# Performance work log

Measured on AMD Instinct MI355X. Metric: run time of the kernel, lower is better.

The kernel has to match this reference:

```python
import jax, jax.numpy as jnp
import numpy as np

N = 1048576        # number of raw proposals
NC = 2             # num classes (source hardcodes self.nc = 2)
CONF_THRES = 0.25  # score_thres
IOU_THRES = 0.45
MAX_WH = 4096.0    # class offset for class-aware NMS (agnostic=False)
MAX_NMS = 30000    # cap on boxes entering NMS
MAX_DET = 300      # cap on detections returned


def setup_inputs() -> dict:
    key = jax.random.key(0)
    k1, k2, k3, k4 = jax.random.split(key, 4)
    xy = jax.random.uniform(k1, (1, N, 2), dtype=jnp.float32) * 640.0          # box centers (pixels)
    wh = jax.random.uniform(k2, (1, N, 2), dtype=jnp.float32) * 98.0 + 2.0     # widths/heights in [2, 100]
    obj = jax.random.uniform(k3, (1, N, 1), dtype=jnp.float32)                 # objectness
    cls = jax.random.uniform(k4, (1, N, NC), dtype=jnp.float32)                # class scores
    prediction = jnp.concatenate([xy, wh, obj, cls], axis=-1)                  # [1, N, 4+1+nc]
    return {"prediction": prediction}


def reference(prediction):
    # Single image (source only ever fills/returns output[0]).
    pred = prediction[0]                        # [N, 7]
    obj = pred[:, 4]                            # objectness
    cls = pred[:, 5:5 + NC] * obj[:, None]      # conf = obj * cls  (nc > 1 branch)
    conf = jnp.max(cls, axis=-1)                # best-class confidence
    j = jnp.argmax(cls, axis=-1)                # best-class index

    # xywh -> xyxy
    xy, wh = pred[:, :2], pred[:, 2:4]
    box = jnp.concatenate([xy - wh * 0.5, xy + wh * 0.5], axis=-1)  # [N, 4]

    # candidate mask: obj > thres (xc) AND best-class conf > thres
    valid = (obj > CONF_THRES) & (conf > CONF_THRES)
    scores = jnp.where(valid, conf, -1.0)

    # n > max_nms: keep top MAX_NMS by confidence (argsort descending truncation)
    top_s, top_i = jax.lax.top_k(scores, MAX_NMS)       # [MAX_NMS]
    box_t = box[top_i]                                   # [MAX_NMS, 4]
    conf_t = conf[top_i]
    j_t = j[top_i]

    # class-aware NMS: offset boxes per class so classes never suppress each other
    boxes_off = box_t + (j_t.astype(box_t.dtype) * MAX_WH)[:, None]
    area = (boxes_off[:, 2] - boxes_off[:, 0]) * (boxes_off[:, 3] - boxes_off[:, 1])

    # Greedy NMS: iteratively select max-score box, suppress IoU > thres.
    # Selecting the argmax each step is equivalent to sorted greedy NMS, and
    # MAX_DET steps yields exactly the first max_det kept indices.
    def step(s, _):
        idx = jnp.argmax(s)
        ok = s[idx] > 0.0                       # any real candidate left?
        b = boxes_off[idx]
        lt = jnp.maximum(b[:2], boxes_off[:, :2])
        rb = jnp.minimum(b[2:], boxes_off[:, 2:])
        inter = jnp.prod(jnp.clip(rb - lt, 0.0), axis=-1)
        iou = inter / (area[idx] + area - inter)
        s = jnp.where(ok & (iou > IOU_THRES), -1.0, s)  # suppress (incl. self, IoU=1)
        return s, (idx, ok)

    _, (sel, ok) = jax.lax.scan(step, top_s, None, length=MAX_DET)

    dets = jnp.concatenate(
        [box_t[sel], conf_t[sel, None], j_t[sel, None].astype(box_t.dtype)], axis=-1
    )                                           # [MAX_DET, 6] = [xyxy, conf, cls]
    dets = dets * ok[:, None].astype(dets.dtype)  # zero out padding rows
    return dets, ok
```

## Files before the change

kernel.cpp:

```cpp
#include <hip/hip_runtime.h>
#include <stdint.h>

#pragma clang fp contract(off)

#define N_ELEM   1048576
#define MAX_NMS  30000
#define MAX_DET  300
#define IOU_T    0.45f
#define CONF_T   0.25f
#define SOA_N    30720
#define KMIN     0xBE800000u
#define EQCAP    2048
#define RPW      16

typedef uint32_t u32;
typedef unsigned long long u64;

#define C_CB   0
#define C_KP   1
#define C_A    2
#define C_NUM  3
#define C_EQC  4

__device__ inline u32 monokey(float s){
  u32 b = __float_as_uint(s);
  return b ^ ((b & 0x80000000u) ? 0xFFFFFFFFu : 0x80000000u);
}
__device__ inline int binOf(u32 k){
  u32 d = (k - KMIN) >> 8;
  return d > 65535u ? 65535 : (int)d;
}
__device__ inline u64 shfl64(u64 v, int src){
  int lo = __shfl((int)(u32)(v & 0xFFFFFFFFull), src);
  int hi = __shfl((int)(u32)(v >> 32), src);
  return ((u64)(u32)hi << 32) | (u32)lo;
}

__global__ void kkeys(const float4* __restrict__ pred4, uint4* __restrict__ keys4,
                      u32* __restrict__ hist){
  int t = blockIdx.x*blockDim.x + threadIdx.x;
  if (t >= N_ELEM/4) return;
  float4 q0 = pred4[(size_t)t*7+0], q1 = pred4[(size_t)t*7+1], q2 = pred4[(size_t)t*7+2];
  float4 q3 = pred4[(size_t)t*7+3], q4 = pred4[(size_t)t*7+4], q5 = pred4[(size_t)t*7+5];
  float4 q6 = pred4[(size_t)t*7+6];
  float f[28];
  f[0]=q0.x; f[1]=q0.y; f[2]=q0.z; f[3]=q0.w;
  f[4]=q1.x; f[5]=q1.y; f[6]=q1.z; f[7]=q1.w;
  f[8]=q2.x; f[9]=q2.y; f[10]=q2.z; f[11]=q2.w;
  f[12]=q3.x; f[13]=q3.y; f[14]=q3.z; f[15]=q3.w;
  f[16]=q4.x; f[17]=q4.y; f[18]=q4.z; f[19]=q4.w;
  f[20]=q5.x; f[21]=q5.y; f[22]=q5.z; f[23]=q5.w;
  f[24]=q6.x; f[25]=q6.y; f[26]=q6.z; f[27]=q6.w;
  u32 kk[4];
  #pragma unroll
  for (int r = 0; r < 4; r++){
    float obj = f[r*7+4], c0 = f[r*7+5], c1 = f[r*7+6];
    float p0 = c0*obj, p1 = c1*obj;
    float conf = fmaxf(p0, p1);
    bool valid = (obj > CONF_T) && (conf > CONF_T);
    float score = valid ? conf : -1.0f;
    kk[r] = monokey(score);
  }
  keys4[t] = make_uint4(kk[0], kk[1], kk[2], kk[3]);
  #pragma unroll
  for (int r = 0; r < 4; r++)
    if (kk[r] > KMIN) atomicAdd(&hist[binOf(kk[r])], 1u);
}

__global__ void kbase(const u32* __restrict__ hist, u32* __restrict__ binBase,
                      u32* __restrict__ ctrl){
  __shared__ u32 s[1024];
  __shared__ int selC;
  __shared__ u32 selAbove;
  __shared__ u32 chunk[64];
  int t = threadIdx.x;
  u32 own = 0;
  #pragma unroll 8
  for (int k = 0; k < 64; k++) own += hist[t*64 + k];
  s[t] = own; __syncthreads();
  for (int off = 1; off < 1024; off <<= 1){
    u32 v = s[t];
    u32 add = (t + off < 1024) ? s[t + off] : 0u;
    __syncthreads();
    s[t] = v + add;
    __syncthreads();
  }
  u32 above = s[t] - own;
  u32 grand = s[0];
  const u32 K = MAX_NMS;
  if (grand >= K){
    if (above < K && K <= above + own){ selC = t; selAbove = above; }
  }
  __syncthreads();
  if (grand >= K && t < 64) chunk[t] = hist[selC*64 + t];
  __syncthreads();
  if (t == 0){
    if (grand < K){
      ctrl[C_CB] = 0xFFFFFFFFu; ctrl[C_KP] = 0; ctrl[C_A] = grand; ctrl[C_NUM] = grand;
    } else {
      u32 cum = selAbove;
      for (int b = 63; b >= 0; b--){
        u32 c = chunk[b];
        if (cum + c >= K){
          ctrl[C_CB] = (u32)(selC*64 + b);
          ctrl[C_KP] = K - cum;
          ctrl[C_A]  = cum;
          ctrl[C_NUM] = K;
          break;
        }
        cum += c;
      }
    }
  }
  u32 run = above;
  for (int b = 63; b >= 0; b--){
    binBase[t*64 + b] = run;
    run += hist[t*64 + b];
  }
}

__global__ void kscatter(const uint4* __restrict__ keys4, const u32* __restrict__ binBase,
                         u32* __restrict__ binCursor, u32* __restrict__ ctrl,
                         u32* __restrict__ binnedKey, u32* __restrict__ binnedIdx,
                         u32* __restrict__ eqKey, u32* __restrict__ eqIdx){
  int t = blockIdx.x*blockDim.x + threadIdx.x;
  if (t >= N_ELEM/4) return;
  int cb = (int)ctrl[C_CB];
  uint4 kv = keys4[t];
  u32 kk[4] = {kv.x, kv.y, kv.z, kv.w};
  #pragma unroll
  for (int r = 0; r < 4; r++){
    u32 k = kk[r];
    if (k <= KMIN) continue;
    int b = binOf(k);
    u32 i = (u32)(t*4 + r);
    if (b > cb){
      u32 pos = binBase[b] + atomicAdd(&binCursor[b], 1u);
      if (pos < MAX_NMS){ binnedKey[pos] = k; binnedIdx[pos] = i; }
    } else if (b == cb){
      u32 e = atomicAdd(&ctrl[C_EQC], 1u);
      if (e < EQCAP){ eqKey[e] = k; eqIdx[e] = i; }
    }
  }
}

__global__ void keq(u32* __restrict__ ctrl, const u32* __restrict__ eqKey,
                    const u32* __restrict__ eqIdx, u32* __restrict__ binnedKey,
                    u32* __restrict__ binnedIdx, u32* __restrict__ binHist){
  u32 Kp = ctrl[C_KP];
  if (Kp == 0) return;
  u32 cb = ctrl[C_CB], A = ctrl[C_A];
  u32 n = ctrl[C_EQC]; if (n > EQCAP) n = EQCAP;
  int lane = threadIdx.x;
  for (u32 e = (u32)lane; e < n; e += 64){
    u32 k = eqKey[e], i = eqIdx[e];
    u32 r = 0;
    for (u32 m = 0; m < n; m++){
      u32 km = eqKey[m], im = eqIdx[m];
      r += (km > k) || (km == k && im < i);
    }
    if (r < Kp){ binnedKey[A + r] = k; binnedIdx[A + r] = i; }
  }
  if (lane == 0) binHist[cb] = Kp;
}

__global__ void krank(const float* __restrict__ pred, const u32* __restrict__ binnedKey,
                      const u32* __restrict__ binnedIdx, const u32* __restrict__ binBase,
                      const u32* __restrict__ binHist, const u32* __restrict__ ctrl,
                      float* __restrict__ soa){
  int p = blockIdx.x*blockDim.x + threadIdx.x;
  int numCand = (int)ctrl[C_NUM];
  if (p >= numCand) return;
  u32 k = binnedKey[p]; u32 i = binnedIdx[p];
  if (i >= N_ELEM) i = 0;
  int b = binOf(k);
  u32 st = binBase[b], cnt = binHist[b];
  u32 r = st;
  for (u32 q = st; q < st + cnt; q++){
    u32 kq = binnedKey[q], iq = binnedIdx[q];
    if (kq > k || (kq == k && iq < i)) r++;
  }
  if (r >= (u32)numCand) return;
  const float* row = pred + (size_t)i*7;
  float x = row[0], y = row[1], w = row[2], hh = row[3];
  float obj = row[4], c0 = row[5], c1 = row[6];
  float p0 = c0*obj, p1 = c1*obj;
  float conf = fmaxf(p0, p1);
  float jf = (p0 >= p1) ? 0.0f : 1.0f;
  float bx1 = x - w*0.5f, by1 = y - hh*0.5f;
  float bx2 = x + w*0.5f, by2 = y + hh*0.5f;
  float off = jf * 4096.0f;
  float ox1 = bx1 + off, oy1 = by1 + off, ox2 = bx2 + off, oy2 = by2 + off;
  float area = (ox2 - ox1) * (oy2 - oy1);
  soa[r + 0*SOA_N] = ox1;  soa[r + 1*SOA_N] = oy1;
  soa[r + 2*SOA_N] = ox2;  soa[r + 3*SOA_N] = oy2;
  soa[r + 4*SOA_N] = area; soa[r + 5*SOA_N] = conf;
  soa[r + 6*SOA_N] = jf;
  soa[r + 7*SOA_N] = bx1;  soa[r + 8*SOA_N] = by1;
  soa[r + 9*SOA_N] = bx2;  soa[r +10*SOA_N] = by2;
}

__global__ void kmask(const float* __restrict__ soa, u64* __restrict__ mask,
                      int W, int WB){
  int lane = threadIdx.x & 63;
  int gw = blockIdx.x*(blockDim.x >> 6) + (threadIdx.x >> 6);
  int nRowG = W / RPW;
  int rowg = gw / WB;
  int w = gw - rowg*WB;
  if (rowg >= nRowG) return;
  if (((w + 1) << 6) <= rowg*RPW) return;
  int j = (w << 6) + lane;
  float cx1 = soa[j], cy1 = soa[j + SOA_N], cx2 = soa[j + 2*SOA_N],
        cy2 = soa[j + 3*SOA_N], ca = soa[j + 4*SOA_N];
  #pragma unroll
  for (int rr = 0; rr < RPW; rr++){
    int i = rowg*RPW + rr;
    if (w < (i >> 6)) continue;
    float rx1 = soa[i], ry1 = soa[i + SOA_N], rx2 = soa[i + 2*SOA_N],
          ry2 = soa[i + 3*SOA_N], ra = soa[i + 4*SOA_N];
    float ltx = fmaxf(rx1, cx1), lty = fmaxf(ry1, cy1);
    float rbx = fminf(rx2, cx2), rby = fminf(ry2, cy2);
    float iw = fmaxf(rbx - ltx, 0.0f), ih = fmaxf(rby - lty, 0.0f);
    float inter = iw * ih;
    float iou = inter / ((ra + ca) - inter);
    u64 m = __ballot(iou > IOU_T);
    if (lane == 0) mask[(size_t)i*WB + w] = m;
  }
}

__global__ void __launch_bounds__(64) kwalk(const float* __restrict__ soa,
                                            const u64* __restrict__ mask,
                                            const u32* __restrict__ ctrl,
                                            float* __restrict__ out, int out_size,
                                            int W){
  __shared__ float kx1[320], ky1[320], kx2[320], ky2[320], ka[320];
  int lane = threadIdx.x;
  for (int o = lane; o < out_size; o += 64) out[o] = 0.0f;
  int numCand = (int)ctrl[C_NUM];
  int WB = W >> 6;
  int lim = numCand < W ? numCand : W;
  int nb = (lim + 63) >> 6;
  u64 rem0 = 0, rem1 = 0;
  int nsel = 0;

  u64 diag = 0;
  if (nb > 0 && lane < lim) diag = mask[(size_t)lane*WB + 0];

  for (int bi = 0; bi < nb && nsel < MAX_DET; bi++){
    u64 remw = (bi < 64) ? shfl64(rem0, bi) : shfl64(rem1, bi - 64);
    u64 w = ~remw;
    int rb = lim - (bi << 6);
    if (rb < 64) w &= ((1ull << rb) - 1ull);
    u64 mydiag = diag;

    u64 diagn = 0;
    int inext = (bi + 1)*64 + lane;
    if (bi + 1 < nb && inext < lim) diagn = mask[(size_t)inext*WB + (bi + 1)];

    u64 sel = 0;
    int room = MAX_DET - nsel;
    while (w){
      int b = (int)__builtin_ctzll(w);
      sel |= (1ull << b);
      if (--room == 0) break;
      u64 rw = shfl64(mydiag, b);
      w &= ~rw;
      w &= ~(1ull << b);
    }
    int cnt = __popcll(sel);

    if (lane < cnt){
      u64 t = sel;
      for (int q = 0; q < lane; q++) t &= t - 1;
      int b = (int)__builtin_ctzll(t);
      int i = (bi << 6) + b;
      int r = nsel + lane;
      kx1[r] = soa[i];            ky1[r] = soa[i + SOA_N];
      kx2[r] = soa[i + 2*SOA_N];  ky2[r] = soa[i + 3*SOA_N];
      ka[r]  = soa[i + 4*SOA_N];
      float* dr = out + r*6;
      dr[0] = soa[i + 7*SOA_N];  dr[1] = soa[i + 8*SOA_N];
      dr[2] = soa[i + 9*SOA_N];  dr[3] = soa[i + 10*SOA_N];
      dr[4] = soa[i + 5*SOA_N];  dr[5] = soa[i + 6*SOA_N];
      out[MAX_DET*6 + r] = 1.0f;
    }
    nsel += cnt;

    u64 s = sel;
    while (s){
      long long ids[8];
      #pragma unroll
      for (int q = 0; q < 8; q++){
        if (s){ ids[q] = (long long)((bi << 6) + __builtin_ctzll(s)); s &= s - 1; }
        else ids[q] = -1;
      }
      u64 a0[8], a1[8];
      #pragma unroll
      for (int q = 0; q < 8; q++){
        a0[q] = 0; a1[q] = 0;
        if (ids[q] >= 0){
          const u64* rp = mask + (size_t)ids[q]*WB;
          if (lane < WB)      a0[q] = rp[lane];
          if (64 + lane < WB) a1[q] = rp[64 + lane];
        }
      }
      #pragma unroll
      for (int q = 0; q < 8; q++){ rem0 |= a0[q]; rem1 |= a1[q]; }
    }
    diag = diagn;
  }

  if (nsel < MAX_DET && numCand > W){
    for (int base = W; base < numCand && nsel < MAX_DET; base += 64){
      int li = base + lane;
      bool has = li < numCand;
      float cox1=0.f,coy1=0.f,cox2=0.f,coy2=0.f,car=1.f,csc=-1.f,ccl=0.f;
      float cbx1=0.f,cby1=0.f,cbx2=0.f,cby2=0.f;
      if (has){
        cox1 = soa[li]; coy1 = soa[li + SOA_N]; cox2 = soa[li + 2*SOA_N];
        coy2 = soa[li + 3*SOA_N]; car = soa[li + 4*SOA_N];
        csc = soa[li + 5*SOA_N]; ccl = soa[li + 6*SOA_N];
        cbx1 = soa[li + 7*SOA_N]; cby1 = soa[li + 8*SOA_N];
        cbx2 = soa[li + 9*SOA_N]; cby2 = soa[li + 10*SOA_N];
      }
      int m = min(64, numCand - base);
      for (int t2 = 0; t2 < m && nsel < MAX_DET; t2++){
        float qx1 = __shfl(cox1, t2), qy1 = __shfl(coy1, t2);
        float qx2 = __shfl(cox2, t2), qy2 = __shfl(coy2, t2);
        float qa  = __shfl(car,  t2);
        bool supp = false;
        #pragma unroll
        for (int q = 0; q < 5; q++){
          int slot = lane + (q << 6);
          if (slot < nsel){
            float ltx = fmaxf(qx1, kx1[slot]), lty = fmaxf(qy1, ky1[slot]);
            float rbx = fminf(qx2, kx2[slot]), rby = fminf(qy2, ky2[slot]);
            float iw = fmaxf(rbx - ltx, 0.0f), ih = fmaxf(rby - lty, 0.0f);
            float inter = iw * ih;
            float iou = inter / ((qa + ka[slot]) - inter);
            supp = supp || (iou > IOU_T);
          }
        }
        if (__any(supp)) continue;
        float bx1 = __shfl(cbx1, t2), by1 = __shfl(cby1, t2);
        float bx2 = __shfl(cbx2, t2), by2 = __shfl(cby2, t2);
        float sc  = __shfl(csc,  t2), cl  = __shfl(ccl,  t2);
        if (lane == 0){
          kx1[nsel] = qx1; ky1[nsel] = qy1; kx2[nsel] = qx2; ky2[nsel] = qy2; ka[nsel] = qa;
          float* dr = out + nsel*6;
          dr[0] = bx1; dr[1] = by1; dr[2] = bx2; dr[3] = by2; dr[4] = sc; dr[5] = cl;
          out[MAX_DET*6 + nsel] = 1.0f;
        }
        nsel++;
      }
    }
  }
}

extern "C" void kernel_launch(void* const* d_in, const int* in_sizes, int n_in,
                              void* d_out, int out_size, void* d_ws, size_t ws_size,
                              hipStream_t stream){
  const float* pred = (const float*)d_in[0];
  float* out = (float*)d_out;
  char* w = (char*)d_ws;

  u32*  keys      = (u32*)(w + 0x000000);
  u32*  hist      = (u32*)(w + 0x400000);
  u32*  binCursor = (u32*)(w + 0x440000);
  u32*  ctrl      = (u32*)(w + 0x480000);
  u32*  binBase   = (u32*)(w + 0x4C0000);
  u32*  eqKey     = (u32*)(w + 0x500000);
  u32*  eqIdx     = (u32*)(w + 0x502000);
  u32*  binnedKey = (u32*)(w + 0x510000);
  u32*  binnedIdx = (u32*)(w + 0x530000);
  float* soa      = (float*)(w + 0x550000);
  u64*  mask      = (u64*)(w + 0x6A0000);

  int W;
  if      (ws_size >= 0xEA0000) W = 8192;
  else if (ws_size >= 0x8A0000) W = 4096;
  else                          W = 2048;
  int WB = W >> 6;

  hipMemsetAsync(hist, 0, 0x80100, stream);

  kkeys   <<<1024, 256, 0, stream>>>((const float4*)pred, (uint4*)keys, hist);
  kbase   <<<1, 1024, 0, stream>>>(hist, binBase, ctrl);
  kscatter<<<1024, 256, 0, stream>>>((const uint4*)keys, binBase, binCursor, ctrl,
                                     binnedKey, binnedIdx, eqKey, eqIdx);
  keq     <<<1, 64, 0, stream>>>(ctrl, eqKey, eqIdx, binnedKey, binnedIdx, hist);
  krank   <<<(MAX_NMS + 255)/256, 256, 0, stream>>>(pred, binnedKey, binnedIdx, binBase,
                                                    hist, ctrl, soa);
  int nwaves = (W/RPW) * WB;
  kmask   <<<(nwaves + 3)/4, 256, 0, stream>>>(soa, mask, W, WB);
  kwalk   <<<1, 64, 0, stream>>>(soa, mask, ctrl, out, out_size, W);
}
```

Before: 296.6 us.

## Parallelize histogram scan, stage key loads via LDS, grid-stride mask, prefetch walk rows

```diff
diff --git a/kernel.cpp b/kernel.cpp
--- a/kernel.cpp
+++ b/kernel.cpp
@@ -36,47 +36,46 @@
   return ((u64)(u32)hi << 32) | (u32)lo;
 }
 
-__global__ void kkeys(const float4* __restrict__ pred4, uint4* __restrict__ keys4,
+__global__ void kkeys(const float4* __restrict__ pred4, u32* __restrict__ keys,
                       u32* __restrict__ hist){
-  int t = blockIdx.x*blockDim.x + threadIdx.x;
-  if (t >= N_ELEM/4) return;
-  float4 q0 = pred4[(size_t)t*7+0], q1 = pred4[(size_t)t*7+1], q2 = pred4[(size_t)t*7+2];
-  float4 q3 = pred4[(size_t)t*7+3], q4 = pred4[(size_t)t*7+4], q5 = pred4[(size_t)t*7+5];
-  float4 q6 = pred4[(size_t)t*7+6];
-  float f[28];
-  f[0]=q0.x; f[1]=q0.y; f[2]=q0.z; f[3]=q0.w;
-  f[4]=q1.x; f[5]=q1.y; f[6]=q1.z; f[7]=q1.w;
-  f[8]=q2.x; f[9]=q2.y; f[10]=q2.z; f[11]=q2.w;
-  f[12]=q3.x; f[13]=q3.y; f[14]=q3.z; f[15]=q3.w;
-  f[16]=q4.x; f[17]=q4.y; f[18]=q4.z; f[19]=q4.w;
-  f[20]=q5.x; f[21]=q5.y; f[22]=q5.z; f[23]=q5.w;
-  f[24]=q6.x; f[25]=q6.y; f[26]=q6.z; f[27]=q6.w;
-  u32 kk[4];
+  __shared__ float lds[1792];
+  int t = threadIdx.x;
+  const float4* src = pred4 + (size_t)blockIdx.x * 448;
+  float4* l4 = (float4*)lds;
   #pragma unroll
-  for (int r = 0; r < 4; r++){
-    float obj = f[r*7+4], c0 = f[r*7+5], c1 = f[r*7+6];
-    float p0 = c0*obj, p1 = c1*obj;
-    float conf = fmaxf(p0, p1);
-    bool valid = (obj > CONF_T) && (conf > CONF_T);
-    float score = valid ? conf : -1.0f;
-    kk[r] = monokey(score);
-  }
-  keys4[t] = make_uint4(kk[0], kk[1], kk[2], kk[3]);
+  for (int k = 0; k < 2; k++){
+    int idx = k*256 + t;
+    if (idx < 448) l4[idx] = src[idx];
+  }
+  __syncthreads();
+  float obj = lds[t*7 + 4], c0 = lds[t*7 + 5], c1 = lds[t*7 + 6];
+  float p0 = c0*obj, p1 = c1*obj;
+  float conf = fmaxf(p0, p1);
+  bool valid = (obj > CONF_T) && (conf > CONF_T);
+  float score = valid ? conf : -1.0f;
+  u32 mk = monokey(score);
+  keys[blockIdx.x*256 + t] = mk;
+  if (mk > KMIN) atomicAdd(&hist[binOf(mk)], 1u);
+}
+
+__global__ void kchunks(const u32* __restrict__ hist, u32* __restrict__ chunkSum){
+  int gw = (blockIdx.x*blockDim.x + threadIdx.x) >> 6;
+  int lane = threadIdx.x & 63;
+  if (gw >= 1024) return;
+  u32 v = hist[gw*64 + lane];
   #pragma unroll
-  for (int r = 0; r < 4; r++)
-    if (kk[r] > KMIN) atomicAdd(&hist[binOf(kk[r])], 1u);
-}
-
-__global__ void kbase(const u32* __restrict__ hist, u32* __restrict__ binBase,
-                      u32* __restrict__ ctrl){
+  for (int off = 32; off > 0; off >>= 1) v += __shfl_down(v, off);
+  if (lane == 0) chunkSum[gw] = v;
+}
+
+__global__ void kpick(const u32* __restrict__ chunkSum, const u32* __restrict__ hist,
+                      u32* __restrict__ chunkAbove, u32* __restrict__ ctrl){
   __shared__ u32 s[1024];
   __shared__ int selC;
   __shared__ u32 selAbove;
   __shared__ u32 chunk[64];
   int t = threadIdx.x;
-  u32 own = 0;
-  #pragma unroll 8
-  for (int k = 0; k < 64; k++) own += hist[t*64 + k];
+  u32 own = chunkSum[t];
   s[t] = own; __syncthreads();
   for (int off = 1; off < 1024; off <<= 1){
     u32 v = s[t];
@@ -86,6 +85,7 @@
     __syncthreads();
   }
   u32 above = s[t] - own;
+  chunkAbove[t] = above;
   u32 grand = s[0];
   const u32 K = MAX_NMS;
   if (grand >= K){
@@ -112,11 +112,21 @@
       }
     }
   }
-  u32 run = above;
-  for (int b = 63; b >= 0; b--){
-    binBase[t*64 + b] = run;
-    run += hist[t*64 + b];
-  }
+}
+
+__global__ void kbinbase(const u32* __restrict__ hist, const u32* __restrict__ chunkAbove,
+                         u32* __restrict__ binBase){
+  int gw = (blockIdx.x*blockDim.x + threadIdx.x) >> 6;
+  int lane = threadIdx.x & 63;
+  if (gw >= 1024) return;
+  u32 v = hist[gw*64 + lane];
+  u32 suf = v;
+  #pragma unroll
+  for (int off = 1; off < 64; off <<= 1){
+    u32 o = __shfl_down(suf, off);
+    suf += (lane + off < 64) ? o : 0u;
+  }
+  binBase[gw*64 + lane] = chunkAbove[gw] + suf - v;
 }
 
 __global__ void kscatter(const uint4* __restrict__ keys4, const u32* __restrict__ binBase,
@@ -201,30 +211,32 @@
 }
 
 __global__ void kmask(const float* __restrict__ soa, u64* __restrict__ mask,
-                      int W, int WB){
+                      int W, int WBsh, int nUnits){
   int lane = threadIdx.x & 63;
-  int gw = blockIdx.x*(blockDim.x >> 6) + (threadIdx.x >> 6);
-  int nRowG = W / RPW;
-  int rowg = gw / WB;
-  int w = gw - rowg*WB;
-  if (rowg >= nRowG) return;
-  if (((w + 1) << 6) <= rowg*RPW) return;
-  int j = (w << 6) + lane;
-  float cx1 = soa[j], cy1 = soa[j + SOA_N], cx2 = soa[j + 2*SOA_N],
-        cy2 = soa[j + 3*SOA_N], ca = soa[j + 4*SOA_N];
-  #pragma unroll
-  for (int rr = 0; rr < RPW; rr++){
-    int i = rowg*RPW + rr;
-    if (w < (i >> 6)) continue;
-    float rx1 = soa[i], ry1 = soa[i + SOA_N], rx2 = soa[i + 2*SOA_N],
-          ry2 = soa[i + 3*SOA_N], ra = soa[i + 4*SOA_N];
-    float ltx = fmaxf(rx1, cx1), lty = fmaxf(ry1, cy1);
-    float rbx = fminf(rx2, cx2), rby = fminf(ry2, cy2);
-    float iw = fmaxf(rbx - ltx, 0.0f), ih = fmaxf(rby - lty, 0.0f);
-    float inter = iw * ih;
-    float iou = inter / ((ra + ca) - inter);
-    u64 m = __ballot(iou > IOU_T);
-    if (lane == 0) mask[(size_t)i*WB + w] = m;
+  int gw = (blockIdx.x*blockDim.x + threadIdx.x) >> 6;
+  int nwaves = (gridDim.x*blockDim.x) >> 6;
+  int WB = 1 << WBsh;
+  for (int u = gw; u < nUnits; u += nwaves){
+    int rowg = u >> WBsh;
+    int w = u & (WB - 1);
+    if (((w + 1) << 6) <= rowg*RPW) continue;
+    int j = (w << 6) + lane;
+    float cx1 = soa[j], cy1 = soa[j + SOA_N], cx2 = soa[j + 2*SOA_N],
+          cy2 = soa[j + 3*SOA_N], ca = soa[j + 4*SOA_N];
+    #pragma unroll
+    for (int rr = 0; rr < RPW; rr++){
+      int i = rowg*RPW + rr;
+      if (w < (i >> 6)) continue;
+      float rx1 = soa[i], ry1 = soa[i + SOA_N], rx2 = soa[i + 2*SOA_N],
+            ry2 = soa[i + 3*SOA_N], ra = soa[i + 4*SOA_N];
+      float ltx = fmaxf(rx1, cx1), lty = fmaxf(ry1, cy1);
+      float rbx = fminf(rx2, cx2), rby = fminf(ry2, cy2);
+      float iw = fmaxf(rbx - ltx, 0.0f), ih = fmaxf(rby - lty, 0.0f);
+      float inter = iw * ih;
+      float iou = inter / ((ra + ca) - inter);
+      u64 m = __ballot(iou > IOU_T);
+      if (lane == 0) mask[(size_t)i*WB + w] = m;
+    }
   }
 }
 
@@ -234,6 +246,7 @@
                                             float* __restrict__ out, int out_size,
                                             int W){
   __shared__ float kx1[320], ky1[320], kx2[320], ky2[320], ka[320];
+  __shared__ u64 dlds[64];
   int lane = threadIdx.x;
   for (int o = lane; o < out_size; o += 64) out[o] = 0.0f;
   int numCand = (int)ctrl[C_NUM];
@@ -251,7 +264,8 @@
     u64 w = ~remw;
     int rb = lim - (bi << 6);
     if (rb < 64) w &= ((1ull << rb) - 1ull);
-    u64 mydiag = diag;
+    dlds[lane] = diag;
+    __syncthreads();
 
     u64 diagn = 0;
     int inext = (bi + 1)*64 + lane;
@@ -263,11 +277,29 @@
       int b = (int)__builtin_ctzll(w);
       sel |= (1ull << b);
       if (--room == 0) break;
-      u64 rw = shfl64(mydiag, b);
+      u64 rw = dlds[b];
       w &= ~rw;
       w &= ~(1ull << b);
     }
     int cnt = __popcll(sel);
+
+    u64 s = sel;
+    long long ids[8];
+    #pragma unroll
+    for (int q = 0; q < 8; q++){
+      if (s){ ids[q] = (long long)((bi << 6) + __builtin_ctzll(s)); s &= s - 1; }
+      else ids[q] = -1;
+    }
+    u64 a0[8], a1[8];
+    #pragma unroll
+    for (int q = 0; q < 8; q++){
+      a0[q] = 0; a1[q] = 0;
+      if (ids[q] >= 0){
+        const u64* rp = mask + (size_t)ids[q]*WB;
+        if (lane < WB)      a0[q] = rp[lane];
+        if (64 + lane < WB) a1[q] = rp[64 + lane];
+      }
+    }
 
     if (lane < cnt){
       u64 t = sel;
@@ -286,28 +318,31 @@
     }
     nsel += cnt;
 
-    u64 s = sel;
+    #pragma unroll
+    for (int q = 0; q < 8; q++){ rem0 |= a0[q]; rem1 |= a1[q]; }
+
     while (s){
-      long long ids[8];
+      long long ids2[8];
       #pragma unroll
       for (int q = 0; q < 8; q++){
-        if (s){ ids[q] = (long long)((bi << 6) + __builtin_ctzll(s)); s &= s - 1; }
-        else ids[q] = -1;
-      }
-      u64 a0[8], a1[8];
+        if (s){ ids2[q] = (long long)((bi << 6) + __builtin_ctzll(s)); s &= s - 1; }
+        else ids2[q] = -1;
+      }
+      u64 b0[8], b1[8];
       #pragma unroll
       for (int q = 0; q < 8; q++){
-        a0[q] = 0; a1[q] = 0;
-        if (ids[q] >= 0){
-          const u64* rp = mask + (size_t)ids[q]*WB;
-          if (lane < WB)      a0[q] = rp[lane];
-          if (64 + lane < WB) a1[q] = rp[64 + lane];
+        b0[q] = 0; b1[q] = 0;
+        if (ids2[q] >= 0){
+          const u64* rp = mask + (size_t)ids2[q]*WB;
+          if (lane < WB)      b0[q] = rp[lane];
+          if (64 + lane < WB) b1[q] = rp[64 + lane];
         }
       }
       #pragma unroll
-      for (int q = 0; q < 8; q++){ rem0 |= a0[q]; rem1 |= a1[q]; }
+      for (int q = 0; q < 8; q++){ rem0 |= b0[q]; rem1 |= b1[q]; }
     }
     diag = diagn;
+    __syncthreads();
   }
 
   if (nsel < MAX_DET && numCand > W){
@@ -364,34 +399,37 @@
   float* out = (float*)d_out;
   char* w = (char*)d_ws;
 
-  u32*  keys      = (u32*)(w + 0x000000);
-  u32*  hist      = (u32*)(w + 0x400000);
-  u32*  binCursor = (u32*)(w + 0x440000);
-  u32*  ctrl      = (u32*)(w + 0x480000);
-  u32*  binBase   = (u32*)(w + 0x4C0000);
-  u32*  eqKey     = (u32*)(w + 0x500000);
-  u32*  eqIdx     = (u32*)(w + 0x502000);
-  u32*  binnedKey = (u32*)(w + 0x510000);
-  u32*  binnedIdx = (u32*)(w + 0x530000);
-  float* soa      = (float*)(w + 0x550000);
-  u64*  mask      = (u64*)(w + 0x6A0000);
-
-  int W;
-  if      (ws_size >= 0xEA0000) W = 8192;
-  else if (ws_size >= 0x8A0000) W = 4096;
-  else                          W = 2048;
-  int WB = W >> 6;
+  u32*  keys       = (u32*)(w + 0x000000);
+  u32*  hist       = (u32*)(w + 0x400000);
+  u32*  binCursor  = (u32*)(w + 0x440000);
+  u32*  ctrl       = (u32*)(w + 0x480000);
+  u32*  chunkSum   = (u32*)(w + 0x484000);
+  u32*  chunkAbove = (u32*)(w + 0x488000);
+  u32*  binBase    = (u32*)(w + 0x4C0000);
+  u32*  eqKey      = (u32*)(w + 0x500000);
+  u32*  eqIdx      = (u32*)(w + 0x502000);
+  u32*  binnedKey  = (u32*)(w + 0x510000);
+  u32*  binnedIdx  = (u32*)(w + 0x530000);
+  float* soa       = (float*)(w + 0x550000);
+  u64*  mask       = (u64*)(w + 0x6A0000);
+
+  int W, WBsh;
+  if      (ws_size >= 0xEA0000){ W = 8192; WBsh = 7; }
+  else if (ws_size >= 0x8A0000){ W = 4096; WBsh = 6; }
+  else                         { W = 2048; WBsh = 5; }
 
   hipMemsetAsync(hist, 0, 0x80100, stream);
 
-  kkeys   <<<1024, 256, 0, stream>>>((const float4*)pred, (uint4*)keys, hist);
-  kbase   <<<1, 1024, 0, stream>>>(hist, binBase, ctrl);
+  kkeys   <<<4096, 256, 0, stream>>>((const float4*)pred, keys, hist);
+  kchunks <<<256, 256, 0, stream>>>(hist, chunkSum);
+  kpick   <<<1, 1024, 0, stream>>>(chunkSum, hist, chunkAbove, ctrl);
+  kbinbase<<<256, 256, 0, stream>>>(hist, chunkAbove, binBase);
   kscatter<<<1024, 256, 0, stream>>>((const uint4*)keys, binBase, binCursor, ctrl,
                                      binnedKey, binnedIdx, eqKey, eqIdx);
   keq     <<<1, 64, 0, stream>>>(ctrl, eqKey, eqIdx, binnedKey, binnedIdx, hist);
   krank   <<<(MAX_NMS + 255)/256, 256, 0, stream>>>(pred, binnedKey, binnedIdx, binBase,
                                                     hist, ctrl, soa);
-  int nwaves = (W/RPW) * WB;
-  kmask   <<<(nwaves + 3)/4, 256, 0, stream>>>(soa, mask, W, WB);
+  int nUnits = (W/RPW) << WBsh;
+  kmask   <<<2048, 256, 0, stream>>>(soa, mask, W, WBsh, nUnits);
   kwalk   <<<1, 64, 0, stream>>>(soa, mask, ctrl, out, out_size, W);
 }
```

Result: faster. 285.9 us (-3.6%).
